# Kernel optimization log

Measured on AMD Instinct MI355X. Metric: run time of the kernel, lower is better.

Reference implementation:

```python
import jax, jax.numpy as jnp
import numpy as np


def setup_inputs() -> dict:
    key = jax.random.key(0)
    k1, k2 = jax.random.split(key)
    B, N, M, C = 32, 4096, 4096, 3
    xyz1 = jax.random.normal(k1, (B, N, C), dtype=jnp.float32)
    xyz2 = jax.random.normal(k2, (B, M, C), dtype=jnp.float32)
    return {"xyz1": xyz1, "xyz2": xyz2}


def _chamfer_l2(xyz1, xyz2):
    # Pairwise squared L2 distances via ||a||^2 + ||b||^2 - 2 a.b  (b n m)
    sq1 = jnp.sum(xyz1 * xyz1, axis=-1)            # [B, N]
    sq2 = jnp.sum(xyz2 * xyz2, axis=-1)            # [B, M]
    cross = jnp.einsum('bnc,bmc->bnm', xyz1, xyz2) # [B, N, M]
    d = sq1[:, :, None] + sq2[:, None, :] - 2.0 * cross
    dist1 = jnp.min(d, axis=2)                     # [B, N] nearest in xyz2
    dist2 = jnp.min(d, axis=1)                     # [B, M] nearest in xyz1
    return jnp.mean(dist1, axis=-1) + jnp.mean(dist2, axis=-1)  # [B]


def reference(xyz1, xyz2):
    return _chamfer_l2(xyz1, xyz2)
```

## Files before the change

### kernel.cpp

```cpp
#include <hip/hip_runtime.h>

typedef _Float16 half8 __attribute__((ext_vector_type(8)));
typedef float floatx16 __attribute__((ext_vector_type(16)));

#define TPB   256
#define RPTS  1024
#define NTILE (RPTS / 32)
#define SMH   (RPTS * 16)

__device__ __forceinline__ unsigned enc(float f) {
    int b = __float_as_int(f);
    return (b >= 0) ? ((unsigned)b | 0x80000000u) : ~(unsigned)b;
}
__device__ __forceinline__ float dec(unsigned k) {
    int b = (k & 0x80000000u) ? (int)(k & 0x7FFFFFFFu) : (int)~k;
    return __int_as_float(b);
}

__global__ __launch_bounds__(256) void pack_frags(const float* __restrict__ src,
                                                  _Float16* __restrict__ dst,
                                                  int npts, int npad) {
    const int b = blockIdx.y;
    const int p = blockIdx.x * 256 + (int)threadIdx.x;
    if (p >= npad) return;
    const int g = p < npts ? p : npts - 1;
    const float* sp = src + ((size_t)b * npts + g) * 3;
    float x = sp[0], y = sp[1], z = sp[2];
    float hq = 0.5f * (x * x + y * y + z * z);
    _Float16 xh = (_Float16)x, yh = (_Float16)y, zh = (_Float16)z;
    _Float16 xl = (_Float16)(x - (float)xh);
    _Float16 yl = (_Float16)(y - (float)yh);
    _Float16 zl = (_Float16)(z - (float)zh);
    _Float16 qh = (_Float16)hq;
    _Float16 ql = (_Float16)(hq - (float)qh);
    const _Float16 hz = (_Float16)0.0f;
    half8 v0, v1;
    v0[0] = xh; v0[1] = xl; v0[2] = xh; v0[3] = yh;
    v0[4] = yl; v0[5] = yh; v0[6] = zh; v0[7] = zl;
    v1[0] = zh; v1[1] = qh; v1[2] = ql; v1[3] = hz;
    v1[4] = hz; v1[5] = hz; v1[6] = hz; v1[7] = hz;
    int t = p >> 5, c = p & 31;
    _Float16* base = dst + (size_t)b * npad * 16 + (size_t)t * 512 + c * 8;
    *(half8*)base         = v0;
    *(half8*)(base + 256) = v1;
}

__global__ __launch_bounds__(TPB, 4) void chamfer_ws(const float* __restrict__ xyz1,
                                                     const float* __restrict__ xyz2,
                                                     const _Float16* __restrict__ frag1,
                                                     const _Float16* __restrict__ frag2,
                                                     unsigned* __restrict__ dist,
                                                     int N, int M, int B,
                                                     int p1pad, int p2pad, int qpad) {
    const int b = blockIdx.y, dir = blockIdx.z;
    const float*    __restrict__ P = dir ? xyz2 + (size_t)b * M * 3 : xyz1 + (size_t)b * N * 3;
    const _Float16* __restrict__ F = dir ? frag1 + (size_t)b * p1pad * 16
                                         : frag2 + (size_t)b * p2pad * 16;
    const int nq    = dir ? M : N;
    const int mdpad = dir ? p1pad : p2pad;

    const int qblk = blockIdx.x >> 1;
    const int s    = blockIdx.x & 1;
    if (qblk * 256 >= nq) return;

    __shared__ __align__(16) _Float16 smB[SMH];

    const int tid = (int)threadIdx.x;
    const int w   = tid >> 6;
    const int l   = tid & 63;
    const int m   = l & 31;
    const int h   = l >> 5;

    const _Float16 hz = (_Float16)0.0f, hone = (_Float16)1.0f;
    const int qb = qblk * 256 + w * 64;

    half8 afr[2];
#pragma unroll
    for (int g = 0; g < 2; ++g) {
        int idx = qb + g * 32 + m;
        int ci  = idx < nq ? idx : nq - 1;
        float x = P[3 * ci], y = P[3 * ci + 1], z = P[3 * ci + 2];
        _Float16 xh = (_Float16)x, yh = (_Float16)y, zh = (_Float16)z;
        _Float16 xl = (_Float16)(x - (float)xh);
        _Float16 yl = (_Float16)(y - (float)yh);
        _Float16 zl = (_Float16)(z - (float)zh);
        half8 a;
        if (h == 0) {
            a[0] = -xh; a[1] = -xh; a[2] = -xl; a[3] = -yh;
            a[4] = -yh; a[5] = -yl; a[6] = -zh; a[7] = -zh;
        } else {
            a[0] = -zl; a[1] = hone; a[2] = hone; a[3] = hz;
            a[4] = hz;  a[5] = hz;   a[6] = hz;  a[7] = hz;
        }
        afr[g] = a;
    }

    float rm[32];
#pragma unroll
    for (int i = 0; i < 32; ++i) rm[i] = 3.0e38f;

    const floatx16 czero = {0.0f, 0.0f, 0.0f, 0.0f, 0.0f, 0.0f, 0.0f, 0.0f,
                            0.0f, 0.0f, 0.0f, 0.0f, 0.0f, 0.0f, 0.0f, 0.0f};
    const int nrounds = mdpad / RPTS;
    const _Float16* bp = smB + h * 256 + m * 8;

    for (int r = s; r < nrounds; r += 2) {
        if (r != s) __syncthreads();
        const int4* __restrict__ gsrc = (const int4*)(F + (size_t)r * SMH);
        int4* __restrict__ ldst = (int4*)smB;
#pragma unroll
        for (int k = 0; k < (SMH * 2 / 16) / TPB; ++k) {
            int c = k * TPB + tid;
            ldst[c] = gsrc[c];
        }
        __syncthreads();

        for (int t = 0; t < NTILE; t += 2) {
            half8 b0 = *(const half8*)(bp + t * 512);
            half8 b1 = *(const half8*)(bp + t * 512 + 512);
            floatx16 d0a = __builtin_amdgcn_mfma_f32_32x32x16_f16(afr[0], b0, czero, 0, 0, 0);
            floatx16 d0b = __builtin_amdgcn_mfma_f32_32x32x16_f16(afr[0], b1, czero, 0, 0, 0);
#pragma unroll
            for (int i = 0; i < 16; ++i)
                rm[i] = fminf(fminf(rm[i], d0a[i]), d0b[i]);
            floatx16 d1a = __builtin_amdgcn_mfma_f32_32x32x16_f16(afr[1], b0, czero, 0, 0, 0);
            floatx16 d1b = __builtin_amdgcn_mfma_f32_32x32x16_f16(afr[1], b1, czero, 0, 0, 0);
#pragma unroll
            for (int i = 0; i < 16; ++i)
                rm[16 + i] = fminf(fminf(rm[16 + i], d1a[i]), d1b[i]);
        }
    }

#pragma unroll
    for (int off = 1; off < 32; off <<= 1) {
#pragma unroll
        for (int i = 0; i < 32; ++i) rm[i] = fminf(rm[i], __shfl_xor(rm[i], off, 64));
    }

    unsigned* dptr = dist + (size_t)(dir * B + b) * qpad;
    if (m < 16) {
        const int reg = (m & 3) + 4 * (m >> 2);
        const int row = 4 * h + (m & 3) + 8 * (m >> 2);
#pragma unroll
        for (int g = 0; g < 2; ++g) {
            int idx = qb + g * 32 + row;
            if (idx < nq) {
                float x = P[3 * idx], y = P[3 * idx + 1], z = P[3 * idx + 2];
                float v = rm[g * 16 + reg] + 0.5f * (x * x + y * y + z * z);
                atomicMin(dptr + idx, enc(v));
            }
        }
    }
}

__global__ __launch_bounds__(256) void reduce_out(const unsigned* __restrict__ dist,
                                                  float* __restrict__ out,
                                                  int N, int M, int B, int qpad) {
    const int b = blockIdx.x;
    const int tid = (int)threadIdx.x;
    float s = 0.0f;
    const unsigned* d0 = dist + (size_t)b * qpad;
    const unsigned* d1 = dist + (size_t)(B + b) * qpad;
    for (int i = tid; i < N; i += 256) s += dec(d0[i]) * (1.0f / (float)N);
    for (int i = tid; i < M; i += 256) s += dec(d1[i]) * (1.0f / (float)M);
#pragma unroll
    for (int off = 32; off > 0; off >>= 1) s += __shfl_down(s, off, 64);
    __shared__ float red[4];
    if ((tid & 63) == 0) red[tid >> 6] = s;
    __syncthreads();
    if (tid == 0) out[b] = 2.0f * (red[0] + red[1] + red[2] + red[3]);
}

__global__ __launch_bounds__(TPB, 4) void chamfer_plain(const float* __restrict__ xyz1,
                                                        const float* __restrict__ xyz2,
                                                        float* __restrict__ out,
                                                        int N, int M) {
    const int b = blockIdx.y, dir = blockIdx.z;
    const float* __restrict__ P = dir ? xyz2 + (size_t)b * M * 3 : xyz1 + (size_t)b * N * 3;
    const float* __restrict__ Q = dir ? xyz1 + (size_t)b * N * 3 : xyz2 + (size_t)b * M * 3;
    const int nq = dir ? M : N;
    const int md = dir ? N : M;
    if ((int)blockIdx.x * TPB >= nq) return;
    __shared__ __align__(16) _Float16 smB[SMH];
    const int tid = (int)threadIdx.x;
    const int w = tid >> 6, l = tid & 63, m = l & 31, h = l >> 5;
    const _Float16 hz = (_Float16)0.0f, hone = (_Float16)1.0f;
    const int qb = blockIdx.x * 256 + w * 64;
    half8 afr[2];
#pragma unroll
    for (int g = 0; g < 2; ++g) {
        int idx = qb + g * 32 + m;
        int ci  = idx < nq ? idx : nq - 1;
        float x = P[3 * ci], y = P[3 * ci + 1], z = P[3 * ci + 2];
        _Float16 xh = (_Float16)x, yh = (_Float16)y, zh = (_Float16)z;
        _Float16 xl = (_Float16)(x - (float)xh);
        _Float16 yl = (_Float16)(y - (float)yh);
        _Float16 zl = (_Float16)(z - (float)zh);
        half8 a;
        if (h == 0) { a[0]=-xh;a[1]=-xh;a[2]=-xl;a[3]=-yh;a[4]=-yh;a[5]=-yl;a[6]=-zh;a[7]=-zh; }
        else        { a[0]=-zl;a[1]=hone;a[2]=hone;a[3]=hz;a[4]=hz;a[5]=hz;a[6]=hz;a[7]=hz; }
        afr[g] = a;
    }
    float rm[32];
#pragma unroll
    for (int i = 0; i < 32; ++i) rm[i] = 3.0e38f;
    const floatx16 czero = {0,0,0,0,0,0,0,0,0,0,0,0,0,0,0,0};
    const int nrounds = (md + RPTS - 1) / RPTS;
    const _Float16* bp = smB + h * 256 + m * 8;
    for (int r = 0; r < nrounds; ++r) {
        if (r) __syncthreads();
#pragma unroll
        for (int k = 0; k < RPTS / TPB; ++k) {
            int j = tid + k * TPB;
            int g = r * RPTS + j;
            g = g < md ? g : md - 1;
            float x = Q[3 * g], y = Q[3 * g + 1], z = Q[3 * g + 2];
            float hq = 0.5f * (x * x + y * y + z * z);
            _Float16 xh = (_Float16)x, yh = (_Float16)y, zh = (_Float16)z;
            _Float16 xl = (_Float16)(x - (float)xh);
            _Float16 yl = (_Float16)(y - (float)yh);
            _Float16 zl = (_Float16)(z - (float)zh);
            _Float16 qh = (_Float16)hq;
            _Float16 ql = (_Float16)(hq - (float)qh);
            int t = j >> 5, c = j & 31;
            half8 v0, v1;
            v0[0]=xh;v0[1]=xl;v0[2]=xh;v0[3]=yh;v0[4]=yl;v0[5]=yh;v0[6]=zh;v0[7]=zl;
            v1[0]=zh;v1[1]=qh;v1[2]=ql;v1[3]=hz;v1[4]=hz;v1[5]=hz;v1[6]=hz;v1[7]=hz;
            *(half8*)&smB[t * 512 + c * 8]       = v0;
            *(half8*)&smB[t * 512 + 256 + c * 8] = v1;
        }
        __syncthreads();
        for (int t = 0; t < NTILE; t += 2) {
            half8 b0 = *(const half8*)(bp + t * 512);
            half8 b1 = *(const half8*)(bp + t * 512 + 512);
            floatx16 d0a = __builtin_amdgcn_mfma_f32_32x32x16_f16(afr[0], b0, czero, 0, 0, 0);
            floatx16 d0b = __builtin_amdgcn_mfma_f32_32x32x16_f16(afr[0], b1, czero, 0, 0, 0);
#pragma unroll
            for (int i = 0; i < 16; ++i) rm[i] = fminf(fminf(rm[i], d0a[i]), d0b[i]);
            floatx16 d1a = __builtin_amdgcn_mfma_f32_32x32x16_f16(afr[1], b0, czero, 0, 0, 0);
            floatx16 d1b = __builtin_amdgcn_mfma_f32_32x32x16_f16(afr[1], b1, czero, 0, 0, 0);
#pragma unroll
            for (int i = 0; i < 16; ++i) rm[16+i] = fminf(fminf(rm[16+i], d1a[i]), d1b[i]);
        }
    }
#pragma unroll
    for (int off = 1; off < 32; off <<= 1) {
#pragma unroll
        for (int i = 0; i < 32; ++i) rm[i] = fminf(rm[i], __shfl_xor(rm[i], off, 64));
    }
    float s = 0.0f;
    if (m < 16) {
        const int reg = (m & 3) + 4 * (m >> 2);
        const int row = 4 * h + (m & 3) + 8 * (m >> 2);
#pragma unroll
        for (int g = 0; g < 2; ++g) {
            int idx = qb + g * 32 + row;
            if (idx < nq) {
                float x = P[3 * idx], y = P[3 * idx + 1], z = P[3 * idx + 2];
                s += rm[g * 16 + reg] + 0.5f * (x * x + y * y + z * z);
            }
        }
    }
#pragma unroll
    for (int off = 32; off > 0; off >>= 1) s += __shfl_down(s, off, 64);
    if (l == 0) atomicAdd(out + b, s * (2.0f / (float)nq));
}

extern "C" void kernel_launch(void* const* d_in, const int* in_sizes, int n_in,
                              void* d_out, int out_size, void* d_ws, size_t ws_size,
                              hipStream_t stream) {
    const float* xyz1 = (const float*)d_in[0];
    const float* xyz2 = (const float*)d_in[1];
    float* out = (float*)d_out;

    const int B = out_size;
    const int N = in_sizes[0] / (3 * B);
    const int M = in_sizes[1] / (3 * B);
    const int qmax = N > M ? N : M;

    const int p1pad = ((N + RPTS - 1) / RPTS) * RPTS;
    const int p2pad = ((M + RPTS - 1) / RPTS) * RPTS;
    const int qpad  = p1pad > p2pad ? p1pad : p2pad;
    const size_t f1bytes = (size_t)B * p1pad * 32;
    const size_t f2bytes = (size_t)B * p2pad * 32;
    const size_t dbytes  = (size_t)2 * B * qpad * sizeof(unsigned);

    if (ws_size >= f1bytes + f2bytes + dbytes) {
        _Float16* frag1 = (_Float16*)d_ws;
        _Float16* frag2 = (_Float16*)((char*)d_ws + f1bytes);
        unsigned* dist  = (unsigned*)((char*)d_ws + f1bytes + f2bytes);

        pack_frags<<<dim3(p1pad / 256, B), dim3(256), 0, stream>>>(xyz1, frag1, N, p1pad);
        pack_frags<<<dim3(p2pad / 256, B), dim3(256), 0, stream>>>(xyz2, frag2, M, p2pad);
        hipMemsetAsync(dist, 0xFF, dbytes, stream);

        dim3 grid(((qmax + 255) / 256) * 2, B, 2);
        chamfer_ws<<<grid, dim3(TPB), 0, stream>>>(xyz1, xyz2, frag1, frag2, dist,
                                                   N, M, B, p1pad, p2pad, qpad);
        reduce_out<<<dim3(B), dim3(256), 0, stream>>>(dist, out, N, M, B, qpad);
    } else {
        hipMemsetAsync(out, 0, (size_t)B * sizeof(float), stream);
        dim3 grid((qmax + 255) / 256, B, 2);
        chamfer_plain<<<grid, dim3(TPB), 0, stream>>>(xyz1, xyz2, out, N, M);
    }
}
```

Measured before the change: 117.9 us.

## Drop split-K atomicMin buffer, fuse reduction into main kernel with smaller query tiles

Each block now covers 128 queries (32 per wave) and sweeps the full reference set itself instead of splitting it across two blocks, so per-query minima are final inside the block. The block then adds its scaled partial mean directly into the output with atomicAdd. This removes the dist buffer, its memset, the atomicMin traffic and the separate reduce kernel. The two pack launches are merged into one that also zeroes the output. Inline asm MFMA with s_nop padding replaces the builtins, and halving the per-wave query count doubles how often each block reloads the reference set into shared memory.

Measured after the change: 147.4 us. 25.0% more time.

```diff
diff --git a/kernel.cpp b/kernel.cpp
--- a/kernel.cpp
+++ b/kernel.cpp
@@ -8,29 +8,35 @@
 #define NTILE (RPTS / 32)
 #define SMH   (RPTS * 16)
 
-__device__ __forceinline__ unsigned enc(float f) {
-    int b = __float_as_int(f);
-    return (b >= 0) ? ((unsigned)b | 0x80000000u) : ~(unsigned)b;
-}
-__device__ __forceinline__ float dec(unsigned k) {
-    int b = (k & 0x80000000u) ? (int)(k & 0x7FFFFFFFu) : (int)~k;
-    return __int_as_float(b);
-}
-
-__global__ __launch_bounds__(256) void pack_frags(const float* __restrict__ src,
-                                                  _Float16* __restrict__ dst,
-                                                  int npts, int npad) {
+__global__ __launch_bounds__(256) void pack_all(const float* __restrict__ xyz1,
+                                                const float* __restrict__ xyz2,
+                                                _Float16* __restrict__ frag1,
+                                                _Float16* __restrict__ frag2,
+                                                float* __restrict__ out,
+                                                int N, int M, int B,
+                                                int p1pad, int p2pad) {
     const int b = blockIdx.y;
+    const int z = blockIdx.z;
     const int p = blockIdx.x * 256 + (int)threadIdx.x;
+
+    if (z == 0 && b == 0 && blockIdx.x == 0) {
+        for (int i = (int)threadIdx.x; i < B; i += 256) out[i] = 0.0f;
+    }
+
+    const int npts = z ? M : N;
+    const int npad = z ? p2pad : p1pad;
     if (p >= npad) return;
+    const float* src = z ? xyz2 : xyz1;
+    _Float16*    dst = z ? frag2 : frag1;
+
     const int g = p < npts ? p : npts - 1;
     const float* sp = src + ((size_t)b * npts + g) * 3;
-    float x = sp[0], y = sp[1], z = sp[2];
-    float hq = 0.5f * (x * x + y * y + z * z);
-    _Float16 xh = (_Float16)x, yh = (_Float16)y, zh = (_Float16)z;
+    float x = sp[0], y = sp[1], zc = sp[2];
+    float hq = 0.5f * (x * x + y * y + zc * zc);
+    _Float16 xh = (_Float16)x, yh = (_Float16)y, zh = (_Float16)zc;
     _Float16 xl = (_Float16)(x - (float)xh);
     _Float16 yl = (_Float16)(y - (float)yh);
-    _Float16 zl = (_Float16)(z - (float)zh);
+    _Float16 zl = (_Float16)(zc - (float)zh);
     _Float16 qh = (_Float16)hq;
     _Float16 ql = (_Float16)(hq - (float)qh);
     const _Float16 hz = (_Float16)0.0f;
@@ -45,13 +51,13 @@
     *(half8*)(base + 256) = v1;
 }
 
-__global__ __launch_bounds__(TPB, 4) void chamfer_ws(const float* __restrict__ xyz1,
-                                                     const float* __restrict__ xyz2,
-                                                     const _Float16* __restrict__ frag1,
-                                                     const _Float16* __restrict__ frag2,
-                                                     unsigned* __restrict__ dist,
-                                                     int N, int M, int B,
-                                                     int p1pad, int p2pad, int qpad) {
+__global__ __launch_bounds__(TPB, 4) void chamfer_main(const float* __restrict__ xyz1,
+                                                       const float* __restrict__ xyz2,
+                                                       const _Float16* __restrict__ frag1,
+                                                       const _Float16* __restrict__ frag2,
+                                                       float* __restrict__ out,
+                                                       int N, int M,
+                                                       int p1pad, int p2pad) {
     const int b = blockIdx.y, dir = blockIdx.z;
     const float*    __restrict__ P = dir ? xyz2 + (size_t)b * M * 3 : xyz1 + (size_t)b * N * 3;
     const _Float16* __restrict__ F = dir ? frag1 + (size_t)b * p1pad * 16
@@ -59,9 +65,7 @@
     const int nq    = dir ? M : N;
     const int mdpad = dir ? p1pad : p2pad;
 
-    const int qblk = blockIdx.x >> 1;
-    const int s    = blockIdx.x & 1;
-    if (qblk * 256 >= nq) return;
+    if ((int)blockIdx.x * 128 >= nq) return;
 
     __shared__ __align__(16) _Float16 smB[SMH];
 
@@ -72,40 +76,35 @@
     const int h   = l >> 5;
 
     const _Float16 hz = (_Float16)0.0f, hone = (_Float16)1.0f;
-    const int qb = qblk * 256 + w * 64;
-
-    half8 afr[2];
-#pragma unroll
-    for (int g = 0; g < 2; ++g) {
-        int idx = qb + g * 32 + m;
+    const int qb = blockIdx.x * 128 + w * 32;
+
+    half8 afr;
+    {
+        int idx = qb + m;
         int ci  = idx < nq ? idx : nq - 1;
         float x = P[3 * ci], y = P[3 * ci + 1], z = P[3 * ci + 2];
         _Float16 xh = (_Float16)x, yh = (_Float16)y, zh = (_Float16)z;
         _Float16 xl = (_Float16)(x - (float)xh);
         _Float16 yl = (_Float16)(y - (float)yh);
         _Float16 zl = (_Float16)(z - (float)zh);
-        half8 a;
         if (h == 0) {
-            a[0] = -xh; a[1] = -xh; a[2] = -xl; a[3] = -yh;
-            a[4] = -yh; a[5] = -yl; a[6] = -zh; a[7] = -zh;
+            afr[0] = -xh; afr[1] = -xh; afr[2] = -xl; afr[3] = -yh;
+            afr[4] = -yh; afr[5] = -yl; afr[6] = -zh; afr[7] = -zh;
         } else {
-            a[0] = -zl; a[1] = hone; a[2] = hone; a[3] = hz;
-            a[4] = hz;  a[5] = hz;   a[6] = hz;  a[7] = hz;
-        }
-        afr[g] = a;
-    }
-
-    float rm[32];
-#pragma unroll
-    for (int i = 0; i < 32; ++i) rm[i] = 3.0e38f;
-
-    const floatx16 czero = {0.0f, 0.0f, 0.0f, 0.0f, 0.0f, 0.0f, 0.0f, 0.0f,
-                            0.0f, 0.0f, 0.0f, 0.0f, 0.0f, 0.0f, 0.0f, 0.0f};
+            afr[0] = -zl; afr[1] = hone; afr[2] = hone; afr[3] = hz;
+            afr[4] = hz;  afr[5] = hz;   afr[6] = hz;  afr[7] = hz;
+        }
+    }
+
+    float rm[16];
+#pragma unroll
+    for (int i = 0; i < 16; ++i) rm[i] = 3.0e38f;
+
     const int nrounds = mdpad / RPTS;
     const _Float16* bp = smB + h * 256 + m * 8;
 
-    for (int r = s; r < nrounds; r += 2) {
-        if (r != s) __syncthreads();
+    for (int r = 0; r < nrounds; ++r) {
+        if (r) __syncthreads();
         const int4* __restrict__ gsrc = (const int4*)(F + (size_t)r * SMH);
         int4* __restrict__ ldst = (int4*)smB;
 #pragma unroll
@@ -118,57 +117,42 @@
         for (int t = 0; t < NTILE; t += 2) {
             half8 b0 = *(const half8*)(bp + t * 512);
             half8 b1 = *(const half8*)(bp + t * 512 + 512);
-            floatx16 d0a = __builtin_amdgcn_mfma_f32_32x32x16_f16(afr[0], b0, czero, 0, 0, 0);
-            floatx16 d0b = __builtin_amdgcn_mfma_f32_32x32x16_f16(afr[0], b1, czero, 0, 0, 0);
+            floatx16 d0, d1;
+            asm("v_mfma_f32_32x32x16_f16 %0, %2, %3, 0\n\t"
+                "v_mfma_f32_32x32x16_f16 %1, %2, %4, 0\n\t"
+                "s_nop 7\n\t"
+                "s_nop 7\n\t"
+                "s_nop 7"
+                : "=&v"(d0), "=&v"(d1)
+                : "v"(afr), "v"(b0), "v"(b1));
 #pragma unroll
             for (int i = 0; i < 16; ++i)
-                rm[i] = fminf(fminf(rm[i], d0a[i]), d0b[i]);
-            floatx16 d1a = __builtin_amdgcn_mfma_f32_32x32x16_f16(afr[1], b0, czero, 0, 0, 0);
-            floatx16 d1b = __builtin_amdgcn_mfma_f32_32x32x16_f16(afr[1], b1, czero, 0, 0, 0);
-#pragma unroll
-            for (int i = 0; i < 16; ++i)
-                rm[16 + i] = fminf(fminf(rm[16 + i], d1a[i]), d1b[i]);
+                rm[i] = fminf(fminf(rm[i], d0[i]), d1[i]);
         }
     }
 
 #pragma unroll
     for (int off = 1; off < 32; off <<= 1) {
 #pragma unroll
-        for (int i = 0; i < 32; ++i) rm[i] = fminf(rm[i], __shfl_xor(rm[i], off, 64));
-    }
-
-    unsigned* dptr = dist + (size_t)(dir * B + b) * qpad;
+        for (int i = 0; i < 16; ++i) rm[i] = fminf(rm[i], __shfl_xor(rm[i], off, 64));
+    }
+
+    float s = 0.0f;
     if (m < 16) {
         const int reg = (m & 3) + 4 * (m >> 2);
         const int row = 4 * h + (m & 3) + 8 * (m >> 2);
-#pragma unroll
-        for (int g = 0; g < 2; ++g) {
-            int idx = qb + g * 32 + row;
-            if (idx < nq) {
-                float x = P[3 * idx], y = P[3 * idx + 1], z = P[3 * idx + 2];
-                float v = rm[g * 16 + reg] + 0.5f * (x * x + y * y + z * z);
-                atomicMin(dptr + idx, enc(v));
-            }
-        }
-    }
-}
-
-__global__ __launch_bounds__(256) void reduce_out(const unsigned* __restrict__ dist,
-                                                  float* __restrict__ out,
-                                                  int N, int M, int B, int qpad) {
-    const int b = blockIdx.x;
-    const int tid = (int)threadIdx.x;
-    float s = 0.0f;
-    const unsigned* d0 = dist + (size_t)b * qpad;
-    const unsigned* d1 = dist + (size_t)(B + b) * qpad;
-    for (int i = tid; i < N; i += 256) s += dec(d0[i]) * (1.0f / (float)N);
-    for (int i = tid; i < M; i += 256) s += dec(d1[i]) * (1.0f / (float)M);
+        const int idx = qb + row;
+        if (idx < nq) {
+            float v = rm[0];
+#pragma unroll
+            for (int r2 = 1; r2 < 16; ++r2) v = (reg == r2) ? rm[r2] : v;
+            float x = P[3 * idx], y = P[3 * idx + 1], z = P[3 * idx + 2];
+            s = v + 0.5f * (x * x + y * y + z * z);
+        }
+    }
 #pragma unroll
     for (int off = 32; off > 0; off >>= 1) s += __shfl_down(s, off, 64);
-    __shared__ float red[4];
-    if ((tid & 63) == 0) red[tid >> 6] = s;
-    __syncthreads();
-    if (tid == 0) out[b] = 2.0f * (red[0] + red[1] + red[2] + red[3]);
+    if (l == 0) atomicAdd(out + b, s * (2.0f / (float)nq));
 }
 
 __global__ __launch_bounds__(TPB, 4) void chamfer_plain(const float* __restrict__ xyz1,
@@ -283,21 +267,17 @@
     const int qpad  = p1pad > p2pad ? p1pad : p2pad;
     const size_t f1bytes = (size_t)B * p1pad * 32;
     const size_t f2bytes = (size_t)B * p2pad * 32;
-    const size_t dbytes  = (size_t)2 * B * qpad * sizeof(unsigned);
-
-    if (ws_size >= f1bytes + f2bytes + dbytes) {
+
+    if (ws_size >= f1bytes + f2bytes) {
         _Float16* frag1 = (_Float16*)d_ws;
         _Float16* frag2 = (_Float16*)((char*)d_ws + f1bytes);
-        unsigned* dist  = (unsigned*)((char*)d_ws + f1bytes + f2bytes);
-
-        pack_frags<<<dim3(p1pad / 256, B), dim3(256), 0, stream>>>(xyz1, frag1, N, p1pad);
-        pack_frags<<<dim3(p2pad / 256, B), dim3(256), 0, stream>>>(xyz2, frag2, M, p2pad);
-        hipMemsetAsync(dist, 0xFF, dbytes, stream);
-
-        dim3 grid(((qmax + 255) / 256) * 2, B, 2);
-        chamfer_ws<<<grid, dim3(TPB), 0, stream>>>(xyz1, xyz2, frag1, frag2, dist,
-                                                   N, M, B, p1pad, p2pad, qpad);
-        reduce_out<<<dim3(B), dim3(256), 0, stream>>>(dist, out, N, M, B, qpad);
+
+        pack_all<<<dim3(qpad / 256, B, 2), dim3(256), 0, stream>>>(
+            xyz1, xyz2, frag1, frag2, out, N, M, B, p1pad, p2pad);
+
+        dim3 grid((qmax + 127) / 128, B, 2);
+        chamfer_main<<<grid, dim3(TPB), 0, stream>>>(xyz1, xyz2, frag1, frag2, out,
+                                                     N, M, p1pad, p2pad);
     } else {
         hipMemsetAsync(out, 0, (size_t)B * sizeof(float), stream);
         dim3 grid((qmax + 255) / 256, B, 2);
```
